# Kernel tuning notes

Hardware: AMD Instinct MI355X
Metric: run time of the kernel (lower is better)

Reference implementation:

```python
import jax, jax.numpy as jnp
import numpy as np

N, D, E, S = 200000, 256, 1000000, 10000

def setup_inputs() -> dict:
    key = jax.random.key(0)
    k1, k2, k3, k4 = jax.random.split(key, 4)
    z = jax.random.normal(k1, (N, D), dtype=jnp.float32)
    attn_w = jax.random.normal(k2, (D,), dtype=jnp.float32) * (1.0 / np.sqrt(D))
    attn_b = jnp.zeros((), dtype=jnp.float32)
    idx = jax.random.randint(k3, (E,), 0, N, dtype=jnp.int64)
    seg = jnp.sort(jax.random.randint(k4, (E,), 0, S, dtype=jnp.int64))
    return {"z": z, "attn_w": attn_w, "attn_b": attn_b, "idx": idx, "seg": seg, "num_segments": S}

def reference(z, attn_w, attn_b, idx, seg, num_segments):
    # Gather ragged groups: sub[e] = z[idx[e]], group id = seg[e]
    sub = z[idx]                                   # [E, D]
    logits = sub @ attn_w + attn_b                 # [E] (nn.Linear(dim,1).squeeze)
    # Segmented, numerically-stable softmax over each group
    m = jax.ops.segment_max(logits, seg, num_segments=num_segments)  # [S]
    m = jnp.where(jnp.isfinite(m), m, 0.0)         # empty segments -> harmless 0
    e = jnp.exp(logits - m[seg])                   # [E]
    den = jax.ops.segment_sum(e, seg, num_segments=num_segments)     # [S]
    w = e / den[seg]                               # [E]
    # Softmax-weighted sum per segment; empty segments yield zeros (matches torch)
    out = jax.ops.segment_sum(sub * w[:, None], seg, num_segments=num_segments)  # [S, D]
    return out
```

## Files before the change

kernel.cpp:

```cpp
#include <hip/hip_runtime.h>
#include <math.h>

#define DDIM 256
#define NWAVES 4

__global__ void seg_offsets_kernel(const int* __restrict__ seg, int E, int S,
                                   int* __restrict__ offs) {
    int i = blockIdx.x * blockDim.x + threadIdx.x;
    if (i > S) return;
    int lo = 0, hi = E;
    while (lo < hi) {
        int mid = (lo + hi) >> 1;
        if (seg[mid] < i) lo = mid + 1; else hi = mid;
    }
    offs[i] = lo;
}

__global__ __launch_bounds__(256)
void segpool_kernel(const float* __restrict__ z,
                    const float* __restrict__ attn_w,
                    const float* __restrict__ attn_b,
                    const int* __restrict__ idx,
                    const int* __restrict__ offs,
                    float* __restrict__ out) {
    const int s     = blockIdx.x;
    const int start = offs[s];
    const int end   = offs[s + 1];
    const int tid   = threadIdx.x;

    if (end <= start) {
        out[(long)s * DDIM + tid] = 0.0f;
        return;
    }

    const int wave = tid >> 6;
    const int lane = tid & 63;
    const float4 wv = ((const float4*)attn_w)[lane];
    const float  b  = attn_b[0];
    const float4* __restrict__ z4 = (const float4*)z;

    float  m = -INFINITY;
    float  l = 0.0f;
    float4 acc = make_float4(0.f, 0.f, 0.f, 0.f);

    for (int e = start + wave; e < end; e += NWAVES) {
        const int   row = idx[e];
        const float4 v  = z4[(long)row * (DDIM / 4) + lane];
        float part = v.x * wv.x + v.y * wv.y + v.z * wv.z + v.w * wv.w;
        #pragma unroll
        for (int sh = 32; sh >= 1; sh >>= 1)
            part += __shfl_xor(part, sh);
        const float logit = part + b;

        const float nm    = fmaxf(m, logit);
        const float alpha = __expf(m - nm);
        const float p     = __expf(logit - nm);
        l      = l * alpha + p;
        acc.x  = acc.x * alpha + p * v.x;
        acc.y  = acc.y * alpha + p * v.y;
        acc.z  = acc.z * alpha + p * v.z;
        acc.w  = acc.w * alpha + p * v.w;
        m      = nm;
    }

    __shared__ float lds_m[NWAVES];
    __shared__ float lds_l[NWAVES];
    __shared__ float lds_acc[NWAVES][DDIM];
    if (lane == 0) { lds_m[wave] = m; lds_l[wave] = l; }
    __syncthreads();

    const float M = fmaxf(fmaxf(lds_m[0], lds_m[1]), fmaxf(lds_m[2], lds_m[3]));
    float den = 0.0f;
    #pragma unroll
    for (int w = 0; w < NWAVES; ++w)
        den += __expf(lds_m[w] - M) * lds_l[w];

    const float scale = __expf(m - M);
    lds_acc[wave][4 * lane + 0] = acc.x * scale;
    lds_acc[wave][4 * lane + 1] = acc.y * scale;
    lds_acc[wave][4 * lane + 2] = acc.z * scale;
    lds_acc[wave][4 * lane + 3] = acc.w * scale;
    __syncthreads();

    const float o = lds_acc[0][tid] + lds_acc[1][tid] +
                    lds_acc[2][tid] + lds_acc[3][tid];
    out[(long)s * DDIM + tid] = o / den;
}

extern "C" void kernel_launch(void* const* d_in, const int* in_sizes, int n_in,
                              void* d_out, int out_size, void* d_ws, size_t ws_size,
                              hipStream_t stream) {
    const float* z      = (const float*)d_in[0];
    const float* attn_w = (const float*)d_in[1];
    const float* attn_b = (const float*)d_in[2];
    const int*   idx    = (const int*)d_in[3];
    const int*   seg    = (const int*)d_in[4];
    float*       out    = (float*)d_out;

    const int E = in_sizes[3];
    const int S = out_size / DDIM;
    int* offs = (int*)d_ws;

    const int threads = 256;
    const int gridA = (S + 1 + threads - 1) / threads;
    seg_offsets_kernel<<<gridA, threads, 0, stream>>>(seg, E, S, offs);
    segpool_kernel<<<S, threads, 0, stream>>>(z, attn_w, attn_b, idx, offs, out);
}
```

Baseline: 408.9 us.

## Precompute per-node logits and use two-pass segmented softmax pooling

```diff
diff --git a/kernel.cpp b/kernel.cpp
--- a/kernel.cpp
+++ b/kernel.cpp
@@ -3,6 +3,7 @@
 
 #define DDIM 256
 #define NWAVES 4
+#define NEG_SENT -1.0e30f
 
 __global__ void seg_offsets_kernel(const int* __restrict__ seg, int E, int S,
                                    int* __restrict__ offs) {
@@ -17,12 +18,29 @@
 }
 
 __global__ __launch_bounds__(256)
-void segpool_kernel(const float* __restrict__ z,
-                    const float* __restrict__ attn_w,
-                    const float* __restrict__ attn_b,
-                    const int* __restrict__ idx,
-                    const int* __restrict__ offs,
-                    float* __restrict__ out) {
+void node_logits_kernel(const float4* __restrict__ z4,
+                        const float* __restrict__ attn_w,
+                        const float* __restrict__ attn_b,
+                        float* __restrict__ logits, int N) {
+    const int wave = threadIdx.x >> 6;
+    const int lane = threadIdx.x & 63;
+    const int row  = blockIdx.x * NWAVES + wave;
+    if (row >= N) return;
+    const float  b  = attn_b[0];
+    const float4 wv = ((const float4*)attn_w)[lane];
+    const float4 v  = z4[(long)row * (DDIM / 4) + lane];
+    float part = v.x * wv.x + v.y * wv.y + v.z * wv.z + v.w * wv.w;
+    #pragma unroll
+    for (int sh = 32; sh >= 1; sh >>= 1) part += __shfl_xor(part, sh);
+    if (lane == 0) logits[row] = part + b;
+}
+
+__global__ __launch_bounds__(256)
+void segpool2_kernel(const float4* __restrict__ z4,
+                     const float* __restrict__ logits,
+                     const int* __restrict__ idx,
+                     const int* __restrict__ offs,
+                     float* __restrict__ out) {
     const int s     = blockIdx.x;
     const int start = offs[s];
     const int end   = offs[s + 1];
@@ -33,55 +51,115 @@
         return;
     }
 
+    const int wave = tid >> 6;
+    const int lane = tid & 63;
+
+    __shared__ float red_m[NWAVES], red_l[NWAVES];
+    __shared__ float s_M, s_invden;
+    __shared__ float lds_acc[NWAVES][DDIM];
+
+    float m = NEG_SENT, l = 0.0f;
+    for (int e = start + tid; e < end; e += 256) {
+        const float lg = logits[idx[e]];
+        const float nm = fmaxf(m, lg);
+        l = l * __expf(m - nm) + __expf(lg - nm);
+        m = nm;
+    }
+    #pragma unroll
+    for (int sh = 32; sh >= 1; sh >>= 1) {
+        const float om = __shfl_xor(m, sh);
+        const float ol = __shfl_xor(l, sh);
+        const float nm = fmaxf(m, om);
+        l = l * __expf(m - nm) + ol * __expf(om - nm);
+        m = nm;
+    }
+    if (lane == 0) { red_m[wave] = m; red_l[wave] = l; }
+    __syncthreads();
+    if (tid == 0) {
+        float M = fmaxf(fmaxf(red_m[0], red_m[1]), fmaxf(red_m[2], red_m[3]));
+        float den = 0.0f;
+        #pragma unroll
+        for (int w = 0; w < NWAVES; ++w) den += red_l[w] * __expf(red_m[w] - M);
+        s_M = M;
+        s_invden = 1.0f / den;
+    }
+    __syncthreads();
+    const float M = s_M;
+    const float invden = s_invden;
+
+    float4 acc = make_float4(0.f, 0.f, 0.f, 0.f);
+    #pragma unroll 4
+    for (int e = start + wave; e < end; e += NWAVES) {
+        const int   row = idx[e];
+        const float p   = __expf(logits[row] - M);
+        const float4 v  = z4[(long)row * (DDIM / 4) + lane];
+        acc.x += p * v.x;
+        acc.y += p * v.y;
+        acc.z += p * v.z;
+        acc.w += p * v.w;
+    }
+
+    lds_acc[wave][4 * lane + 0] = acc.x;
+    lds_acc[wave][4 * lane + 1] = acc.y;
+    lds_acc[wave][4 * lane + 2] = acc.z;
+    lds_acc[wave][4 * lane + 3] = acc.w;
+    __syncthreads();
+
+    const float o = lds_acc[0][tid] + lds_acc[1][tid] +
+                    lds_acc[2][tid] + lds_acc[3][tid];
+    out[(long)s * DDIM + tid] = o * invden;
+}
+
+__global__ __launch_bounds__(256)
+void segpool_fused_kernel(const float* __restrict__ z,
+                          const float* __restrict__ attn_w,
+                          const float* __restrict__ attn_b,
+                          const int* __restrict__ idx,
+                          const int* __restrict__ offs,
+                          float* __restrict__ out) {
+    const int s     = blockIdx.x;
+    const int start = offs[s];
+    const int end   = offs[s + 1];
+    const int tid   = threadIdx.x;
+    if (end <= start) { out[(long)s * DDIM + tid] = 0.0f; return; }
     const int wave = tid >> 6;
     const int lane = tid & 63;
     const float4 wv = ((const float4*)attn_w)[lane];
     const float  b  = attn_b[0];
     const float4* __restrict__ z4 = (const float4*)z;
-
-    float  m = -INFINITY;
-    float  l = 0.0f;
+    float  m = NEG_SENT, l = 0.0f;
     float4 acc = make_float4(0.f, 0.f, 0.f, 0.f);
-
     for (int e = start + wave; e < end; e += NWAVES) {
         const int   row = idx[e];
         const float4 v  = z4[(long)row * (DDIM / 4) + lane];
         float part = v.x * wv.x + v.y * wv.y + v.z * wv.z + v.w * wv.w;
         #pragma unroll
-        for (int sh = 32; sh >= 1; sh >>= 1)
-            part += __shfl_xor(part, sh);
+        for (int sh = 32; sh >= 1; sh >>= 1) part += __shfl_xor(part, sh);
         const float logit = part + b;
-
         const float nm    = fmaxf(m, logit);
         const float alpha = __expf(m - nm);
         const float p     = __expf(logit - nm);
-        l      = l * alpha + p;
-        acc.x  = acc.x * alpha + p * v.x;
-        acc.y  = acc.y * alpha + p * v.y;
-        acc.z  = acc.z * alpha + p * v.z;
-        acc.w  = acc.w * alpha + p * v.w;
-        m      = nm;
-    }
-
-    __shared__ float lds_m[NWAVES];
-    __shared__ float lds_l[NWAVES];
+        l = l * alpha + p;
+        acc.x = acc.x * alpha + p * v.x;
+        acc.y = acc.y * alpha + p * v.y;
+        acc.z = acc.z * alpha + p * v.z;
+        acc.w = acc.w * alpha + p * v.w;
+        m = nm;
+    }
+    __shared__ float lds_m[NWAVES], lds_l[NWAVES];
     __shared__ float lds_acc[NWAVES][DDIM];
     if (lane == 0) { lds_m[wave] = m; lds_l[wave] = l; }
     __syncthreads();
-
     const float M = fmaxf(fmaxf(lds_m[0], lds_m[1]), fmaxf(lds_m[2], lds_m[3]));
     float den = 0.0f;
     #pragma unroll
-    for (int w = 0; w < NWAVES; ++w)
-        den += __expf(lds_m[w] - M) * lds_l[w];
-
+    for (int w = 0; w < NWAVES; ++w) den += __expf(lds_m[w] - M) * lds_l[w];
     const float scale = __expf(m - M);
     lds_acc[wave][4 * lane + 0] = acc.x * scale;
     lds_acc[wave][4 * lane + 1] = acc.y * scale;
     lds_acc[wave][4 * lane + 2] = acc.z * scale;
     lds_acc[wave][4 * lane + 3] = acc.w * scale;
     __syncthreads();
-
     const float o = lds_acc[0][tid] + lds_acc[1][tid] +
                     lds_acc[2][tid] + lds_acc[3][tid];
     out[(long)s * DDIM + tid] = o / den;
@@ -99,10 +177,26 @@
 
     const int E = in_sizes[3];
     const int S = out_size / DDIM;
-    int* offs = (int*)d_ws;
+    const int N = in_sizes[0] / DDIM;
 
     const int threads = 256;
     const int gridA = (S + 1 + threads - 1) / threads;
+
+    int* offs = (int*)d_ws;
+    const size_t offs_bytes = (((size_t)(S + 1) * sizeof(int)) + 255) & ~(size_t)255;
+    const size_t need = offs_bytes + (size_t)N * sizeof(float);
+
     seg_offsets_kernel<<<gridA, threads, 0, stream>>>(seg, E, S, offs);
-    segpool_kernel<<<S, threads, 0, stream>>>(z, attn_w, attn_b, idx, offs, out);
-}
+
+    if (ws_size >= need) {
+        float* logits = (float*)((char*)d_ws + offs_bytes);
+        const int gridB = (N + NWAVES - 1) / NWAVES;
+        node_logits_kernel<<<gridB, threads, 0, stream>>>(
+            (const float4*)z, attn_w, attn_b, logits, N);
+        segpool2_kernel<<<S, threads, 0, stream>>>(
+            (const float4*)z, logits, idx, offs, out);
+    } else {
+        segpool_fused_kernel<<<S, threads, 0, stream>>>(
+            z, attn_w, attn_b, idx, offs, out);
+    }
+}
```

New measurement: 441.9 us. 8.1% more time.
